# Optimization experiments

Hardware: AMD Instinct MI355X
Metric: run time of the kernel (lower is better)

## Reference

```python
import jax, jax.numpy as jnp
import numpy as np
from jax import lax

D_MODEL = 1024
D_FF = 4096
NUM_EXPERTS = 24
TOP_K = 2


def setup_inputs() -> dict:
    key = jax.random.key(0)
    ks = jax.random.split(key, 7)
    s1 = 1.0 / np.sqrt(D_MODEL)
    s2 = 1.0 / np.sqrt(D_FF)
    x = jax.random.normal(ks[0], (2, 1024, D_MODEL), dtype=jnp.float32)
    gate_w = jax.random.uniform(ks[1], (D_MODEL, NUM_EXPERTS), jnp.float32, -s1, s1)
    gate_b = jax.random.uniform(ks[2], (NUM_EXPERTS,), jnp.float32, -s1, s1)
    w1 = jax.random.uniform(ks[3], (NUM_EXPERTS, D_MODEL, D_FF), jnp.float32, -s1, s1)
    b1 = jax.random.uniform(ks[4], (NUM_EXPERTS, D_FF), jnp.float32, -s1, s1)
    w2 = jax.random.uniform(ks[5], (NUM_EXPERTS, D_FF, D_MODEL), jnp.float32, -s2, s2)
    b2 = jax.random.uniform(ks[6], (NUM_EXPERTS, D_MODEL), jnp.float32, -s2, s2)
    return {"x": x, "gate_w": gate_w, "gate_b": gate_b, "w1": w1, "b1": b1, "w2": w2, "b2": b2}


def reference(x, gate_w, gate_b, w1, b1, w2, b2):
    # x: [B, S, D]
    gate_scores = jnp.einsum('bsd,de->bse', x, gate_w) + gate_b            # [B,S,E]
    topk_val, topk_idx = lax.top_k(gate_scores, TOP_K)                      # [B,S,K]
    sparse_gates = jax.nn.softmax(topk_val, axis=-1)                        # [B,S,K]
    # dense combine weights: w[b,s,e] = sum_k sg[b,s,k] * (idx[b,s,k]==e)
    combine = jnp.sum(jax.nn.one_hot(topk_idx, NUM_EXPERTS, dtype=x.dtype)
                      * sparse_gates[..., None], axis=-2)                   # [B,S,E]
    # grouped FFN: run all tokens through all experts, zero-weighted combine
    h = jax.nn.gelu(jnp.einsum('bsd,edf->besf', x, w1)
                    + b1[None, :, None, :], approximate=False)              # [B,E,S,F]
    y = jnp.einsum('besf,efd->besd', h, w2) + b2[None, :, None, :]          # [B,E,S,D]
    out = jnp.einsum('bse,besd->bsd', combine, y)                           # [B,S,D]
    return out + x
```

## Files before the change

### kernel.cpp

```cpp
#include <hip/hip_runtime.h>
#include <hip/hip_bf16.h>
#include <math.h>

typedef unsigned short u16;
typedef unsigned int u32;
typedef short s8v __attribute__((ext_vector_type(8)));
typedef float f4v __attribute__((ext_vector_type(4)));

#define D_MODEL 1024
#define D_FF    4096
#define NE      24
#define T_TOT   2048
#define SLOTS   (2*T_TOT)
#define CAP     2048
#define BM      64
#define BN      128
#define BK      32
#define MAXT    96
#define LDA     40

#define OFF_GATES   0
#define OFF_COUNTS  (OFF_GATES + T_TOT*2*4)
#define OFF_NT      (OFF_COUNTS + 128)
#define OFF_MT      (OFF_NT + 128)
#define OFF_TLIST   (OFF_MT + 512)
#define OFF_H       (OFF_TLIST + NE*CAP*4)
#define OFF_Y       (OFF_H + (size_t)SLOTS*D_FF*2)

__device__ __forceinline__ u16 f2bf(float f) {
    u32 u = __builtin_bit_cast(u32, f);
    u32 r = (u + 0x7FFF + ((u >> 16) & 1)) >> 16;
    return (u16)r;
}
__device__ __forceinline__ float bf2f(u16 u) {
    u32 x = ((u32)u) << 16;
    return __builtin_bit_cast(float, x);
}

__global__ void zero_kern(int* __restrict__ counts) {
    if (threadIdx.x < NE) counts[threadIdx.x] = 0;
}

__global__ void gate_kern(const float* __restrict__ x, const float* __restrict__ gw,
                          const float* __restrict__ gb, float* __restrict__ gates,
                          int* __restrict__ counts, int* __restrict__ tlist) {
    int t = blockIdx.x;
    int lane = threadIdx.x;
    float acc[NE];
#pragma unroll
    for (int e = 0; e < NE; e++) acc[e] = 0.f;
    const float* xr = x + (size_t)t * D_MODEL;
#pragma unroll 4
    for (int i = 0; i < D_MODEL / 64; i++) {
        int d = lane + i * 64;
        float xv = xr[d];
        const float* g = gw + (size_t)d * NE;
#pragma unroll
        for (int e = 0; e < NE; e++) acc[e] = fmaf(xv, g[e], acc[e]);
    }
#pragma unroll
    for (int m = 1; m < 64; m <<= 1) {
#pragma unroll
        for (int e = 0; e < NE; e++) acc[e] += __shfl_xor(acc[e], m, 64);
    }
    if (lane == 0) {
        float v0 = -1e30f, v1 = -1e30f;
        int i0 = 0, i1 = 0;
#pragma unroll
        for (int e = 0; e < NE; e++) {
            float v = acc[e] + gb[e];
            if (v > v0) { v1 = v0; i1 = i0; v0 = v; i0 = e; }
            else if (v > v1) { v1 = v; i1 = e; }
        }
        float e1 = __expf(v1 - v0);
        float inv = 1.f / (1.f + e1);
        gates[t * 2 + 0] = inv;
        gates[t * 2 + 1] = e1 * inv;
        int p0 = atomicAdd(&counts[i0], 1);
        tlist[i0 * CAP + p0] = t * 2 + 0;
        int p1 = atomicAdd(&counts[i1], 1);
        tlist[i1 * CAP + p1] = t * 2 + 1;
    }
}

__global__ void sched_kern(const int* __restrict__ counts, int* __restrict__ ntl,
                           int* __restrict__ mtl, int* __restrict__ tlist) {
    int tid = threadIdx.x;
    for (int idx = tid; idx < NE * 64; idx += 256) {
        int e = idx >> 6, j = idx & 63;
        int c = counts[e];
        int cr = ((c + BM - 1) / BM) * BM;
        if (c + j < cr) tlist[e * CAP + c + j] = -1;
    }
    if (tid == 0) {
        int tot = 0;
        for (int e = 0; e < NE; e++) {
            int nt = (counts[e] + BM - 1) / BM;
            for (int i = 0; i < nt; i++) mtl[tot++] = (e << 16) | i;
        }
        ntl[0] = tot;
    }
}

__global__ __launch_bounds__(256) void gemm1_kern(
    const float* __restrict__ x, const float* __restrict__ w1, const float* __restrict__ b1,
    const int* __restrict__ ntl, const int* __restrict__ mtl, const int* __restrict__ tlist,
    u16* __restrict__ h) {
    int mt = blockIdx.y;
    if (mt >= ntl[0]) return;
    int ent = mtl[mt];
    int e = ent >> 16, tile = ent & 0xFFFF;
    int f0 = blockIdx.x * BN;
    const int* tl = tlist + e * CAP + tile * BM;

    __shared__ u16 As[BM * LDA];
    __shared__ u16 Bs[BN * LDA];

    int tid = threadIdx.x;
    int arow = tid >> 2, akc = (tid & 3) * 8;
    int aslot = tl[arow];
    const float* ap = x + (size_t)(aslot >> 1) * D_MODEL + akc;
    int bn4 = (tid & 31) * 4, bkb = (tid >> 5) * 4;
    const float* bp = w1 + (size_t)e * D_MODEL * D_FF + f0 + bn4;

    int wave = tid >> 6, lane = tid & 63;
    int quad = lane >> 4, l16 = lane & 15;

    f4v acc[4][2];
#pragma unroll
    for (int i = 0; i < 4; i++)
#pragma unroll
        for (int j = 0; j < 2; j++) acc[i][j] = (f4v){0.f, 0.f, 0.f, 0.f};

    for (int k0 = 0; k0 < D_MODEL; k0 += BK) {
        ushort4 av0 = {0, 0, 0, 0}, av1 = {0, 0, 0, 0};
        if (aslot >= 0) {
            float4 a0 = *(const float4*)(ap + k0);
            float4 a1 = *(const float4*)(ap + k0 + 4);
            av0 = (ushort4){f2bf(a0.x), f2bf(a0.y), f2bf(a0.z), f2bf(a0.w)};
            av1 = (ushort4){f2bf(a1.x), f2bf(a1.y), f2bf(a1.z), f2bf(a1.w)};
        }
        *(ushort4*)&As[arow * LDA + akc] = av0;
        *(ushort4*)&As[arow * LDA + akc + 4] = av1;

        float4 q0 = *(const float4*)(bp + (size_t)(k0 + bkb + 0) * D_FF);
        float4 q1 = *(const float4*)(bp + (size_t)(k0 + bkb + 1) * D_FF);
        float4 q2 = *(const float4*)(bp + (size_t)(k0 + bkb + 2) * D_FF);
        float4 q3 = *(const float4*)(bp + (size_t)(k0 + bkb + 3) * D_FF);
        const float* p0 = (const float*)&q0;
        const float* p1 = (const float*)&q1;
        const float* p2 = (const float*)&q2;
        const float* p3 = (const float*)&q3;
#pragma unroll
        for (int j = 0; j < 4; j++) {
            uint2 wv;
            wv.x = (u32)f2bf(p0[j]) | ((u32)f2bf(p1[j]) << 16);
            wv.y = (u32)f2bf(p2[j]) | ((u32)f2bf(p3[j]) << 16);
            *(uint2*)&Bs[(bn4 + j) * LDA + bkb] = wv;
        }
        __syncthreads();

        s8v af[4], bfr[2];
#pragma unroll
        for (int mf = 0; mf < 4; mf++)
            af[mf] = *(const s8v*)&As[(mf * 16 + l16) * LDA + quad * 8];
#pragma unroll
        for (int nf = 0; nf < 2; nf++)
            bfr[nf] = *(const s8v*)&Bs[(wave * 32 + nf * 16 + l16) * LDA + quad * 8];
#pragma unroll
        for (int mf = 0; mf < 4; mf++)
#pragma unroll
            for (int nf = 0; nf < 2; nf++)
                acc[mf][nf] = __builtin_amdgcn_mfma_f32_16x16x32_bf16(af[mf], bfr[nf], acc[mf][nf], 0, 0, 0);
        __syncthreads();
    }

#pragma unroll
    for (int mf = 0; mf < 4; mf++) {
        int rowb = mf * 16 + quad * 4;
#pragma unroll
        for (int r = 0; r < 4; r++) {
            int slot = tl[rowb + r];
            if (slot < 0) continue;
#pragma unroll
            for (int nf = 0; nf < 2; nf++) {
                int f = f0 + wave * 32 + nf * 16 + l16;
                float v = acc[mf][nf][r] + b1[e * D_FF + f];
                float g = 0.5f * v * (1.f + erff(v * 0.70710678118654752f));
                h[(size_t)slot * D_FF + f] = f2bf(g);
            }
        }
    }
}

__global__ __launch_bounds__(256) void gemm2_kern(
    const u16* __restrict__ h, const float* __restrict__ w2, const float* __restrict__ b2,
    const int* __restrict__ ntl, const int* __restrict__ mtl, const int* __restrict__ tlist,
    float* __restrict__ y) {
    int mt = blockIdx.y;
    if (mt >= ntl[0]) return;
    int ent = mtl[mt];
    int e = ent >> 16, tile = ent & 0xFFFF;
    int d0 = blockIdx.x * BN;
    const int* tl = tlist + e * CAP + tile * BM;

    __shared__ u16 As[BM * LDA];
    __shared__ u16 Bs[BN * LDA];

    int tid = threadIdx.x;
    int arow = tid >> 2, akc = (tid & 3) * 8;
    int aslot = tl[arow];
    const u16* ap = h + (size_t)aslot * D_FF + akc;
    int bn4 = (tid & 31) * 4, bkb = (tid >> 5) * 4;
    const float* bp = w2 + (size_t)e * D_FF * D_MODEL + d0 + bn4;

    int wave = tid >> 6, lane = tid & 63;
    int quad = lane >> 4, l16 = lane & 15;

    f4v acc[4][2];
#pragma unroll
    for (int i = 0; i < 4; i++)
#pragma unroll
        for (int j = 0; j < 2; j++) acc[i][j] = (f4v){0.f, 0.f, 0.f, 0.f};

    for (int k0 = 0; k0 < D_FF; k0 += BK) {
        uint4 av = {0u, 0u, 0u, 0u};
        if (aslot >= 0) av = *(const uint4*)(ap + k0);
        *(uint4*)&As[arow * LDA + akc] = av;

        float4 q0 = *(const float4*)(bp + (size_t)(k0 + bkb + 0) * D_MODEL);
        float4 q1 = *(const float4*)(bp + (size_t)(k0 + bkb + 1) * D_MODEL);
        float4 q2 = *(const float4*)(bp + (size_t)(k0 + bkb + 2) * D_MODEL);
        float4 q3 = *(const float4*)(bp + (size_t)(k0 + bkb + 3) * D_MODEL);
        const float* p0 = (const float*)&q0;
        const float* p1 = (const float*)&q1;
        const float* p2 = (const float*)&q2;
        const float* p3 = (const float*)&q3;
#pragma unroll
        for (int j = 0; j < 4; j++) {
            uint2 wv;
            wv.x = (u32)f2bf(p0[j]) | ((u32)f2bf(p1[j]) << 16);
            wv.y = (u32)f2bf(p2[j]) | ((u32)f2bf(p3[j]) << 16);
            *(uint2*)&Bs[(bn4 + j) * LDA + bkb] = wv;
        }
        __syncthreads();

        s8v af[4], bfr[2];
#pragma unroll
        for (int mf = 0; mf < 4; mf++)
            af[mf] = *(const s8v*)&As[(mf * 16 + l16) * LDA + quad * 8];
#pragma unroll
        for (int nf = 0; nf < 2; nf++)
            bfr[nf] = *(const s8v*)&Bs[(wave * 32 + nf * 16 + l16) * LDA + quad * 8];
#pragma unroll
        for (int mf = 0; mf < 4; mf++)
#pragma unroll
            for (int nf = 0; nf < 2; nf++)
                acc[mf][nf] = __builtin_amdgcn_mfma_f32_16x16x32_bf16(af[mf], bfr[nf], acc[mf][nf], 0, 0, 0);
        __syncthreads();
    }

#pragma unroll
    for (int mf = 0; mf < 4; mf++) {
        int rowb = mf * 16 + quad * 4;
#pragma unroll
        for (int r = 0; r < 4; r++) {
            int slot = tl[rowb + r];
            if (slot < 0) continue;
#pragma unroll
            for (int nf = 0; nf < 2; nf++) {
                int d = d0 + wave * 32 + nf * 16 + l16;
                y[(size_t)slot * D_MODEL + d] = acc[mf][nf][r] + b2[e * D_MODEL + d];
            }
        }
    }
}

__global__ void combine_kern(const float* __restrict__ x, const float* __restrict__ y,
                             const float* __restrict__ gates, float* __restrict__ out) {
    int gid = blockIdx.x * blockDim.x + threadIdx.x;
    int t = gid >> 7;
    int c = (gid & 127) << 3;
    float g0 = gates[t * 2 + 0], g1 = gates[t * 2 + 1];
    const float* xp = x + (size_t)t * D_MODEL + c;
    const float* ap = y + (size_t)(t * 2 + 0) * D_MODEL + c;
    const float* bp = y + (size_t)(t * 2 + 1) * D_MODEL + c;
    float* op = out + (size_t)t * D_MODEL + c;
    float4 x0 = *(const float4*)(xp), x1 = *(const float4*)(xp + 4);
    float4 a0 = *(const float4*)(ap), a1 = *(const float4*)(ap + 4);
    float4 b0 = *(const float4*)(bp), b1v = *(const float4*)(bp + 4);
    float4 o0, o1;
    o0.x = x0.x + g0 * a0.x + g1 * b0.x;
    o0.y = x0.y + g0 * a0.y + g1 * b0.y;
    o0.z = x0.z + g0 * a0.z + g1 * b0.z;
    o0.w = x0.w + g0 * a0.w + g1 * b0.w;
    o1.x = x1.x + g0 * a1.x + g1 * b1v.x;
    o1.y = x1.y + g0 * a1.y + g1 * b1v.y;
    o1.z = x1.z + g0 * a1.z + g1 * b1v.z;
    o1.w = x1.w + g0 * a1.w + g1 * b1v.w;
    *(float4*)(op) = o0;
    *(float4*)(op + 4) = o1;
}

extern "C" void kernel_launch(void* const* d_in, const int* in_sizes, int n_in,
                              void* d_out, int out_size, void* d_ws, size_t ws_size,
                              hipStream_t stream) {
    const float* x  = (const float*)d_in[0];
    const float* gw = (const float*)d_in[1];
    const float* gb = (const float*)d_in[2];
    const float* w1 = (const float*)d_in[3];
    const float* b1 = (const float*)d_in[4];
    const float* w2 = (const float*)d_in[5];
    const float* b2 = (const float*)d_in[6];
    float* out = (float*)d_out;

    char* ws = (char*)d_ws;
    float* gates = (float*)(ws + OFF_GATES);
    int* counts  = (int*)(ws + OFF_COUNTS);
    int* ntl     = (int*)(ws + OFF_NT);
    int* mtl     = (int*)(ws + OFF_MT);
    int* tlist   = (int*)(ws + OFF_TLIST);
    u16* h       = (u16*)(ws + OFF_H);
    float* y     = (float*)(ws + OFF_Y);

    zero_kern<<<1, 64, 0, stream>>>(counts);
    gate_kern<<<T_TOT, 64, 0, stream>>>(x, gw, gb, gates, counts, tlist);
    sched_kern<<<1, 256, 0, stream>>>(counts, ntl, mtl, tlist);
    gemm1_kern<<<dim3(D_FF / BN, MAXT), 256, 0, stream>>>(x, w1, b1, ntl, mtl, tlist, h);
    gemm2_kern<<<dim3(D_MODEL / BN, MAXT), 256, 0, stream>>>(h, w2, b2, ntl, mtl, tlist, y);
    combine_kern<<<(T_TOT * D_MODEL / 8) / 256, 256, 0, stream>>>(x, y, gates, out);
}
```

Before: 995.0 us.

## Enlarge expert M-tiles, pre-convert x to bf16, use direct-to-LDS loads with swizzle

Grows each expert row tile from 64 to 192 tokens (three 64-row subtiles per block), so each fp32 weight tile loaded and converted to bf16 is reused across three times as many tokens. Adds a kernel that converts x to bf16 once, so the GEMM A tiles can be fetched with global_load_lds straight into an XOR-swizzled shared layout instead of a padded one. Also uses the packed v_cvt_pk_bf16_f32 instruction for conversions. In exchange it pads each expert's token list up to a multiple of 192, which means more wasted rows, and it raises accumulator register pressure while leaving fewer blocks in the grid.

```diff
diff --git a/kernel.cpp b/kernel.cpp
--- a/kernel.cpp
+++ b/kernel.cpp
@@ -12,33 +12,49 @@
 #define NE      24
 #define T_TOT   2048
 #define SLOTS   (2*T_TOT)
-#define CAP     2048
-#define BM      64
+#define CAP     2112
+#define SBM     192
+#define MT      3
 #define BN      128
 #define BK      32
-#define MAXT    96
-#define LDA     40
+#define MAXT    48
 
 #define OFF_GATES   0
 #define OFF_COUNTS  (OFF_GATES + T_TOT*2*4)
 #define OFF_NT      (OFF_COUNTS + 128)
 #define OFF_MT      (OFF_NT + 128)
 #define OFF_TLIST   (OFF_MT + 512)
-#define OFF_H       (OFF_TLIST + NE*CAP*4)
+#define OFF_XB      (OFF_TLIST + NE*CAP*4)
+#define OFF_H       (OFF_XB + (size_t)T_TOT*D_MODEL*2)
 #define OFF_Y       (OFF_H + (size_t)SLOTS*D_FF*2)
 
-__device__ __forceinline__ u16 f2bf(float f) {
-    u32 u = __builtin_bit_cast(u32, f);
-    u32 r = (u + 0x7FFF + ((u >> 16) & 1)) >> 16;
-    return (u16)r;
-}
-__device__ __forceinline__ float bf2f(u16 u) {
-    u32 x = ((u32)u) << 16;
-    return __builtin_bit_cast(float, x);
+typedef __attribute__((address_space(1))) unsigned int AS1_u32;
+typedef __attribute__((address_space(3))) unsigned int AS3_u32;
+
+__device__ __forceinline__ void gload16(const void* g, void* l) {
+    __builtin_amdgcn_global_load_lds((const AS1_u32*)g, (AS3_u32*)l, 16, 0, 0);
+}
+
+__device__ __forceinline__ u32 cvt_pk(float a, float b) {
+    u32 r;
+    asm("v_cvt_pk_bf16_f32 %0, %1, %2" : "=v"(r) : "v"(a), "v"(b));
+    return r;
 }
 
 __global__ void zero_kern(int* __restrict__ counts) {
     if (threadIdx.x < NE) counts[threadIdx.x] = 0;
+}
+
+__global__ void xcvt_kern(const float* __restrict__ x, u16* __restrict__ xb) {
+    int gid = blockIdx.x * 256 + threadIdx.x;
+    const float4* xp = (const float4*)(x + (size_t)gid * 8);
+    float4 a = xp[0], b = xp[1];
+    uint4 o;
+    o.x = cvt_pk(a.x, a.y);
+    o.y = cvt_pk(a.z, a.w);
+    o.z = cvt_pk(b.x, b.y);
+    o.w = cvt_pk(b.z, b.w);
+    ((uint4*)xb)[gid] = o;
 }
 
 __global__ void gate_kern(const float* __restrict__ x, const float* __restrict__ gw,
@@ -86,67 +102,72 @@
 __global__ void sched_kern(const int* __restrict__ counts, int* __restrict__ ntl,
                            int* __restrict__ mtl, int* __restrict__ tlist) {
     int tid = threadIdx.x;
-    for (int idx = tid; idx < NE * 64; idx += 256) {
-        int e = idx >> 6, j = idx & 63;
+    for (int idx = tid; idx < NE * SBM; idx += 256) {
+        int e = idx / SBM, j = idx % SBM;
         int c = counts[e];
-        int cr = ((c + BM - 1) / BM) * BM;
+        int cr = ((c + SBM - 1) / SBM) * SBM;
         if (c + j < cr) tlist[e * CAP + c + j] = -1;
     }
     if (tid == 0) {
         int tot = 0;
         for (int e = 0; e < NE; e++) {
-            int nt = (counts[e] + BM - 1) / BM;
+            int nt = (counts[e] + SBM - 1) / SBM;
             for (int i = 0; i < nt; i++) mtl[tot++] = (e << 16) | i;
         }
         ntl[0] = tot;
     }
 }
 
+
 __global__ __launch_bounds__(256) void gemm1_kern(
-    const float* __restrict__ x, const float* __restrict__ w1, const float* __restrict__ b1,
+    const u16* __restrict__ xb, const float* __restrict__ w1, const float* __restrict__ b1,
     const int* __restrict__ ntl, const int* __restrict__ mtl, const int* __restrict__ tlist,
     u16* __restrict__ h) {
-    int mt = blockIdx.y;
-    if (mt >= ntl[0]) return;
-    int ent = mtl[mt];
+    int mtile = blockIdx.y;
+    if (mtile >= ntl[0]) return;
+    int ent = mtl[mtile];
     int e = ent >> 16, tile = ent & 0xFFFF;
     int f0 = blockIdx.x * BN;
-    const int* tl = tlist + e * CAP + tile * BM;
-
-    __shared__ u16 As[BM * LDA];
-    __shared__ u16 Bs[BN * LDA];
+    const int* tl = tlist + e * CAP + tile * SBM;
+
+    __shared__ u16 As[SBM * 32];
+    __shared__ u16 Bs[BN * 32];
 
     int tid = threadIdx.x;
-    int arow = tid >> 2, akc = (tid & 3) * 8;
-    int aslot = tl[arow];
-    const float* ap = x + (size_t)(aslot >> 1) * D_MODEL + akc;
+    int wave = tid >> 6, lane = tid & 63, quad = lane >> 4, l16 = lane & 15;
+
+    const u16* asrc[3];
+#pragma unroll
+    for (int c = 0; c < 3; c++) {
+        int i = c * 256 + tid;
+        int row = i >> 2, pc = i & 3;
+        int sl = tl[row]; if (sl < 0) sl = 0;
+        int lc = pc ^ ((row >> 2) & 3);
+        asrc[c] = xb + (size_t)(sl >> 1) * D_MODEL + lc * 8;
+    }
+
     int bn4 = (tid & 31) * 4, bkb = (tid >> 5) * 4;
     const float* bp = w1 + (size_t)e * D_MODEL * D_FF + f0 + bn4;
-
-    int wave = tid >> 6, lane = tid & 63;
-    int quad = lane >> 4, l16 = lane & 15;
-
-    f4v acc[4][2];
-#pragma unroll
-    for (int i = 0; i < 4; i++)
-#pragma unroll
-        for (int j = 0; j < 2; j++) acc[i][j] = (f4v){0.f, 0.f, 0.f, 0.f};
+    int bwoff = bn4 * 32 + (((bkb >> 3) ^ (tid & 3)) << 3) + (bkb & 7);
+
+    int pco = (quad ^ ((l16 >> 2) & 3)) << 3;
+
+    f4v acc[MT][4][2];
+#pragma unroll
+    for (int m = 0; m < MT; m++)
+#pragma unroll
+        for (int i = 0; i < 4; i++)
+#pragma unroll
+            for (int j = 0; j < 2; j++) acc[m][i][j] = (f4v){0.f, 0.f, 0.f, 0.f};
 
     for (int k0 = 0; k0 < D_MODEL; k0 += BK) {
-        ushort4 av0 = {0, 0, 0, 0}, av1 = {0, 0, 0, 0};
-        if (aslot >= 0) {
-            float4 a0 = *(const float4*)(ap + k0);
-            float4 a1 = *(const float4*)(ap + k0 + 4);
-            av0 = (ushort4){f2bf(a0.x), f2bf(a0.y), f2bf(a0.z), f2bf(a0.w)};
-            av1 = (ushort4){f2bf(a1.x), f2bf(a1.y), f2bf(a1.z), f2bf(a1.w)};
-        }
-        *(ushort4*)&As[arow * LDA + akc] = av0;
-        *(ushort4*)&As[arow * LDA + akc + 4] = av1;
-
         float4 q0 = *(const float4*)(bp + (size_t)(k0 + bkb + 0) * D_FF);
         float4 q1 = *(const float4*)(bp + (size_t)(k0 + bkb + 1) * D_FF);
         float4 q2 = *(const float4*)(bp + (size_t)(k0 + bkb + 2) * D_FF);
         float4 q3 = *(const float4*)(bp + (size_t)(k0 + bkb + 3) * D_FF);
+#pragma unroll
+        for (int c = 0; c < 3; c++)
+            gload16(asrc[c] + k0, &As[(c * 256 + tid) * 8]);
         const float* p0 = (const float*)&q0;
         const float* p1 = (const float*)&q1;
         const float* p2 = (const float*)&q2;
@@ -154,84 +175,104 @@
 #pragma unroll
         for (int j = 0; j < 4; j++) {
             uint2 wv;
-            wv.x = (u32)f2bf(p0[j]) | ((u32)f2bf(p1[j]) << 16);
-            wv.y = (u32)f2bf(p2[j]) | ((u32)f2bf(p3[j]) << 16);
-            *(uint2*)&Bs[(bn4 + j) * LDA + bkb] = wv;
+            wv.x = cvt_pk(p0[j], p1[j]);
+            wv.y = cvt_pk(p2[j], p3[j]);
+            *(uint2*)&Bs[bwoff + j * 32] = wv;
         }
         __syncthreads();
 
-        s8v af[4], bfr[2];
-#pragma unroll
-        for (int mf = 0; mf < 4; mf++)
-            af[mf] = *(const s8v*)&As[(mf * 16 + l16) * LDA + quad * 8];
+        s8v bfr[2];
 #pragma unroll
         for (int nf = 0; nf < 2; nf++)
-            bfr[nf] = *(const s8v*)&Bs[(wave * 32 + nf * 16 + l16) * LDA + quad * 8];
-#pragma unroll
-        for (int mf = 0; mf < 4; mf++)
-#pragma unroll
-            for (int nf = 0; nf < 2; nf++)
-                acc[mf][nf] = __builtin_amdgcn_mfma_f32_16x16x32_bf16(af[mf], bfr[nf], acc[mf][nf], 0, 0, 0);
+            bfr[nf] = *(const s8v*)&Bs[(wave * 32 + nf * 16 + l16) * 32 + pco];
+#pragma unroll
+        for (int m = 0; m < MT; m++) {
+            s8v af[4];
+#pragma unroll
+            for (int mf = 0; mf < 4; mf++)
+                af[mf] = *(const s8v*)&As[(m * 64 + mf * 16 + l16) * 32 + pco];
+#pragma unroll
+            for (int mf = 0; mf < 4; mf++)
+#pragma unroll
+                for (int nf = 0; nf < 2; nf++)
+                    acc[m][mf][nf] = __builtin_amdgcn_mfma_f32_16x16x32_bf16(af[mf], bfr[nf], acc[m][mf][nf], 0, 0, 0);
+        }
         __syncthreads();
     }
 
-#pragma unroll
-    for (int mf = 0; mf < 4; mf++) {
-        int rowb = mf * 16 + quad * 4;
-#pragma unroll
-        for (int r = 0; r < 4; r++) {
-            int slot = tl[rowb + r];
-            if (slot < 0) continue;
-#pragma unroll
-            for (int nf = 0; nf < 2; nf++) {
-                int f = f0 + wave * 32 + nf * 16 + l16;
-                float v = acc[mf][nf][r] + b1[e * D_FF + f];
-                float g = 0.5f * v * (1.f + erff(v * 0.70710678118654752f));
-                h[(size_t)slot * D_FF + f] = f2bf(g);
+    float bb[2];
+#pragma unroll
+    for (int nf = 0; nf < 2; nf++) bb[nf] = b1[e * D_FF + f0 + wave * 32 + nf * 16 + l16];
+#pragma unroll
+    for (int m = 0; m < MT; m++)
+#pragma unroll
+        for (int mf = 0; mf < 4; mf++) {
+            int rowb = m * 64 + mf * 16 + quad * 4;
+#pragma unroll
+            for (int r = 0; r < 4; r++) {
+                int slot = tl[rowb + r];
+                if (slot < 0) continue;
+                float v0 = acc[m][mf][0][r] + bb[0];
+                float v1 = acc[m][mf][1][r] + bb[1];
+                float g0 = 0.5f * v0 * (1.f + erff(v0 * 0.70710678118654752f));
+                float g1 = 0.5f * v1 * (1.f + erff(v1 * 0.70710678118654752f));
+                u32 pr = cvt_pk(g0, g1);
+                u16* hp = h + (size_t)slot * D_FF + f0 + wave * 32 + l16;
+                hp[0]  = (u16)pr;
+                hp[16] = (u16)(pr >> 16);
             }
         }
-    }
 }
 
 __global__ __launch_bounds__(256) void gemm2_kern(
     const u16* __restrict__ h, const float* __restrict__ w2, const float* __restrict__ b2,
     const int* __restrict__ ntl, const int* __restrict__ mtl, const int* __restrict__ tlist,
     float* __restrict__ y) {
-    int mt = blockIdx.y;
-    if (mt >= ntl[0]) return;
-    int ent = mtl[mt];
+    int mtile = blockIdx.y;
+    if (mtile >= ntl[0]) return;
+    int ent = mtl[mtile];
     int e = ent >> 16, tile = ent & 0xFFFF;
     int d0 = blockIdx.x * BN;
-    const int* tl = tlist + e * CAP + tile * BM;
-
-    __shared__ u16 As[BM * LDA];
-    __shared__ u16 Bs[BN * LDA];
+    const int* tl = tlist + e * CAP + tile * SBM;
+
+    __shared__ u16 As[SBM * 32];
+    __shared__ u16 Bs[BN * 32];
 
     int tid = threadIdx.x;
-    int arow = tid >> 2, akc = (tid & 3) * 8;
-    int aslot = tl[arow];
-    const u16* ap = h + (size_t)aslot * D_FF + akc;
+    int wave = tid >> 6, lane = tid & 63, quad = lane >> 4, l16 = lane & 15;
+
+    const u16* asrc[3];
+#pragma unroll
+    for (int c = 0; c < 3; c++) {
+        int i = c * 256 + tid;
+        int row = i >> 2, pc = i & 3;
+        int sl = tl[row]; if (sl < 0) sl = 0;
+        int lc = pc ^ ((row >> 2) & 3);
+        asrc[c] = h + (size_t)sl * D_FF + lc * 8;
+    }
+
     int bn4 = (tid & 31) * 4, bkb = (tid >> 5) * 4;
     const float* bp = w2 + (size_t)e * D_FF * D_MODEL + d0 + bn4;
-
-    int wave = tid >> 6, lane = tid & 63;
-    int quad = lane >> 4, l16 = lane & 15;
-
-    f4v acc[4][2];
-#pragma unroll
-    for (int i = 0; i < 4; i++)
-#pragma unroll
-        for (int j = 0; j < 2; j++) acc[i][j] = (f4v){0.f, 0.f, 0.f, 0.f};
+    int bwoff = bn4 * 32 + (((bkb >> 3) ^ (tid & 3)) << 3) + (bkb & 7);
+
+    int pco = (quad ^ ((l16 >> 2) & 3)) << 3;
+
+    f4v acc[MT][4][2];
+#pragma unroll
+    for (int m = 0; m < MT; m++)
+#pragma unroll
+        for (int i = 0; i < 4; i++)
+#pragma unroll
+            for (int j = 0; j < 2; j++) acc[m][i][j] = (f4v){0.f, 0.f, 0.f, 0.f};
 
     for (int k0 = 0; k0 < D_FF; k0 += BK) {
-        uint4 av = {0u, 0u, 0u, 0u};
-        if (aslot >= 0) av = *(const uint4*)(ap + k0);
-        *(uint4*)&As[arow * LDA + akc] = av;
-
         float4 q0 = *(const float4*)(bp + (size_t)(k0 + bkb + 0) * D_MODEL);
         float4 q1 = *(const float4*)(bp + (size_t)(k0 + bkb + 1) * D_MODEL);
         float4 q2 = *(const float4*)(bp + (size_t)(k0 + bkb + 2) * D_MODEL);
         float4 q3 = *(const float4*)(bp + (size_t)(k0 + bkb + 3) * D_MODEL);
+#pragma unroll
+        for (int c = 0; c < 3; c++)
+            gload16(asrc[c] + k0, &As[(c * 256 + tid) * 8]);
         const float* p0 = (const float*)&q0;
         const float* p1 = (const float*)&q1;
         const float* p2 = (const float*)&q2;
@@ -239,41 +280,48 @@
 #pragma unroll
         for (int j = 0; j < 4; j++) {
             uint2 wv;
-            wv.x = (u32)f2bf(p0[j]) | ((u32)f2bf(p1[j]) << 16);
-            wv.y = (u32)f2bf(p2[j]) | ((u32)f2bf(p3[j]) << 16);
-            *(uint2*)&Bs[(bn4 + j) * LDA + bkb] = wv;
+            wv.x = cvt_pk(p0[j], p1[j]);
+            wv.y = cvt_pk(p2[j], p3[j]);
+            *(uint2*)&Bs[bwoff + j * 32] = wv;
         }
         __syncthreads();
 
-        s8v af[4], bfr[2];
-#pragma unroll
-        for (int mf = 0; mf < 4; mf++)
-            af[mf] = *(const s8v*)&As[(mf * 16 + l16) * LDA + quad * 8];
+        s8v bfr[2];
 #pragma unroll
         for (int nf = 0; nf < 2; nf++)
-            bfr[nf] = *(const s8v*)&Bs[(wave * 32 + nf * 16 + l16) * LDA + quad * 8];
-#pragma unroll
-        for (int mf = 0; mf < 4; mf++)
-#pragma unroll
-            for (int nf = 0; nf < 2; nf++)
-                acc[mf][nf] = __builtin_amdgcn_mfma_f32_16x16x32_bf16(af[mf], bfr[nf], acc[mf][nf], 0, 0, 0);
+            bfr[nf] = *(const s8v*)&Bs[(wave * 32 + nf * 16 + l16) * 32 + pco];
+#pragma unroll
+        for (int m = 0; m < MT; m++) {
+            s8v af[4];
+#pragma unroll
+            for (int mf = 0; mf < 4; mf++)
+                af[mf] = *(const s8v*)&As[(m * 64 + mf * 16 + l16) * 32 + pco];
+#pragma unroll
+            for (int mf = 0; mf < 4; mf++)
+#pragma unroll
+                for (int nf = 0; nf < 2; nf++)
+                    acc[m][mf][nf] = __builtin_amdgcn_mfma_f32_16x16x32_bf16(af[mf], bfr[nf], acc[m][mf][nf], 0, 0, 0);
+        }
         __syncthreads();
     }
 
-#pragma unroll
-    for (int mf = 0; mf < 4; mf++) {
-        int rowb = mf * 16 + quad * 4;
-#pragma unroll
-        for (int r = 0; r < 4; r++) {
-            int slot = tl[rowb + r];
-            if (slot < 0) continue;
-#pragma unroll
-            for (int nf = 0; nf < 2; nf++) {
-                int d = d0 + wave * 32 + nf * 16 + l16;
-                y[(size_t)slot * D_MODEL + d] = acc[mf][nf][r] + b2[e * D_MODEL + d];
+    float bb[2];
+#pragma unroll
+    for (int nf = 0; nf < 2; nf++) bb[nf] = b2[e * D_MODEL + d0 + wave * 32 + nf * 16 + l16];
+#pragma unroll
+    for (int m = 0; m < MT; m++)
+#pragma unroll
+        for (int mf = 0; mf < 4; mf++) {
+            int rowb = m * 64 + mf * 16 + quad * 4;
+#pragma unroll
+            for (int r = 0; r < 4; r++) {
+                int slot = tl[rowb + r];
+                if (slot < 0) continue;
+                float* yp = y + (size_t)slot * D_MODEL + d0 + wave * 32 + l16;
+                yp[0]  = acc[m][mf][0][r] + bb[0];
+                yp[16] = acc[m][mf][1][r] + bb[1];
             }
         }
-    }
 }
 
 __global__ void combine_kern(const float* __restrict__ x, const float* __restrict__ y,
@@ -320,13 +368,15 @@
     int* ntl     = (int*)(ws + OFF_NT);
     int* mtl     = (int*)(ws + OFF_MT);
     int* tlist   = (int*)(ws + OFF_TLIST);
+    u16* xb      = (u16*)(ws + OFF_XB);
     u16* h       = (u16*)(ws + OFF_H);
     float* y     = (float*)(ws + OFF_Y);
 
     zero_kern<<<1, 64, 0, stream>>>(counts);
+    xcvt_kern<<<T_TOT * D_MODEL / (8 * 256), 256, 0, stream>>>(x, xb);
     gate_kern<<<T_TOT, 64, 0, stream>>>(x, gw, gb, gates, counts, tlist);
     sched_kern<<<1, 256, 0, stream>>>(counts, ntl, mtl, tlist);
-    gemm1_kern<<<dim3(D_FF / BN, MAXT), 256, 0, stream>>>(x, w1, b1, ntl, mtl, tlist, h);
+    gemm1_kern<<<dim3(D_FF / BN, MAXT), 256, 0, stream>>>(xb, w1, b1, ntl, mtl, tlist, h);
     gemm2_kern<<<dim3(D_MODEL / BN, MAXT), 256, 0, stream>>>(h, w2, b2, ntl, mtl, tlist, y);
     combine_kern<<<(T_TOT * D_MODEL / 8) / 256, 256, 0, stream>>>(x, y, gates, out);
 }
```

Measured after the change: 981.5 us. No clear change (-1.4%).
